# Kernel tuning notes

Hardware: AMD Instinct MI355X
Metric: run time of the kernel (lower is better)

## Reference

```python
import jax, jax.numpy as jnp
import numpy as np

MB, NK, DM, DT = 4096, 8, 1024, 128
EPS = 1e-3  # LayerNormalization eps, added to sigma OUTSIDE sqrt


def setup_inputs() -> dict:
    key = jax.random.key(0)
    ks = jax.random.split(key, 7)
    xav = lambda fan_in, fan_out: (2.0 / (fan_in + fan_out)) ** 0.5
    return {
        "q": jax.random.normal(ks[0], (MB, NK, DM), jnp.float32),
        "k": jax.random.normal(ks[1], (MB, NK, DM), jnp.float32),
        "v": jax.random.normal(ks[2], (MB, NK, DM), jnp.float32),
        "w_qs": jax.random.normal(ks[3], (NK, DM, DT), jnp.float32) * xav(DM, DT),
        "w_ks": jax.random.normal(ks[4], (NK, DM, DT), jnp.float32) * xav(DM, DT),
        "w_vs": jax.random.normal(ks[5], (NK, DM, DT), jnp.float32) * xav(DM, DT),
        # torch Linear: weight [out, in] = [NK*DM, NK*DT]
        "proj_w": jax.random.normal(ks[6], (NK * DM, NK * DT), jnp.float32) * xav(NK * DT, NK * DM),
        "proj_b": jnp.zeros((NK * DM,), jnp.float32),
        "gamma": jnp.ones((DM,), jnp.float32),
        "beta": jnp.zeros((DM,), jnp.float32),
    }


def reference(q, k, v, w_qs, w_ks, w_vs, proj_w, proj_b, gamma, beta):
    mb, nk, dm = q.shape
    dt = w_qs.shape[-1]
    residual = v

    # torch: q.view(n_kernel, mb, d_model) on contiguous [mb, nk, dm] == raw reshape
    q_s = jnp.einsum('nbd,ndt->nbt', q.reshape(nk, mb, dm), w_qs)  # [nk, mb, dt]
    k_s = jnp.einsum('nbd,ndt->nbt', k.reshape(nk, mb, dm), w_ks)
    v_s = jnp.einsum('nbd,ndt->nbt', v.reshape(nk, mb, dm), w_vs)

    # ScaledDotProductAttention on [nk*mb, 1, dt] -> scores [.,1,1]; softmax over
    # a singleton dim is identically 1, so output == v_s (faithful to source).
    temper = np.float32(np.sqrt(dm))
    scores = jnp.sum(q_s * k_s, axis=-1) / temper            # [nk, mb]
    attn = jax.nn.softmax(scores[:, :, None, None], axis=-1)  # [nk, mb, 1, 1] == 1.0
    out = attn[..., 0] * v_s                                  # [nk, mb, dt]
    attns = attn.reshape(nk * mb, 1, 1)

    # torch .view(mb, nk*dt) on the [nk, mb, dt]-contiguous buffer (raw reshape)
    outputs = out.reshape(mb, nk * dt)
    outputs = outputs @ proj_w.T + proj_b                     # [mb, nk*dm]
    z = outputs.reshape(mb, nk, dm) + residual

    # custom LayerNormalization: unbiased std, eps outside sqrt
    mu = jnp.mean(z, axis=-1, keepdims=True)
    sigma = jnp.std(z, axis=-1, keepdims=True, ddof=1)
    output = (z - mu) / (sigma + EPS) * gamma + beta
    return (output, attns)
```

## Files before the change

### kernel.cpp

```cpp
#include <hip/hip_runtime.h>
#include <cstdint>
#include <cstddef>

#define MB_   4096
#define NK_   8
#define DM_   1024
#define DT_   128

typedef __bf16 bf16;
typedef __bf16 bf16x8 __attribute__((ext_vector_type(8)));
typedef __bf16 bf16x4 __attribute__((ext_vector_type(4)));
typedef float  f32x4  __attribute__((ext_vector_type(4)));

__device__ __forceinline__ void gload_lds16(const void* g, void* l) {
  __builtin_amdgcn_global_load_lds(
      (__attribute__((address_space(1))) void*)g,
      (__attribute__((address_space(3))) void*)l,
      16, 0, 0);
}

__device__ __forceinline__ int hsw(int r) { return (r ^ (r >> 2)) & 3; }

__global__ void prep_pw_kernel(const float* __restrict__ pw, bf16* __restrict__ pwb) {
  size_t i = ((size_t)blockIdx.x * 256 + threadIdx.x) * 4;
  float4 f = *(const float4*)&pw[i];
  bf16x4 o = { (bf16)f.x, (bf16)f.y, (bf16)f.z, (bf16)f.w };
  *(bf16x4*)&pwb[i] = o;
}

__global__ void prep_wvt_kernel(const float* __restrict__ wvs, bf16* __restrict__ wvt) {
  int o = blockIdx.x * 256 + threadIdx.x;
  int d = o & 1023;
  int t = (o >> 10) & 127;
  int n = o >> 17;
  wvt[o] = (bf16)wvs[(size_t)n * 131072 + (size_t)d * 128 + t];
}

__global__ void fill_attns_kernel(float* __restrict__ out) {
  out[(size_t)33554432 + blockIdx.x * 256 + threadIdx.x] = 1.0f;
}

__global__ __launch_bounds__(256, 2) void gemm1_kernel(
    const float* __restrict__ vflat, const bf16* __restrict__ WvT,
    bf16* __restrict__ A2)
{
  __shared__ __align__(16) bf16 As[64 * 32];
  __shared__ __align__(16) bf16 Bs[128 * 32];
  const int tid  = threadIdx.x;
  const int wave = tid >> 6, lane = tid & 63;
  const int wm = wave >> 1, wn = wave & 1;
  const int n  = blockIdx.y;
  const int b0 = blockIdx.x * 64;

  const int r  = tid >> 2;
  const int hr = hsw(r);
  const int cs = (tid & 3) ^ hr;

  const float* ag = vflat + ((size_t)(n * MB_ + b0 + r)) * 1024 + (tid & 3) * 8;
  bf16* awr = As + r * 32 + cs * 8;
  const bf16* bg = WvT + (size_t)n * 131072 + (size_t)r * 1024 + cs * 8;
  char* bsb = (char*)Bs + wave * 1024;

  f32x4 acc[2][4] = {};
  const int krow = lane & 15;
  const int cch  = lane >> 4;
  const int swoff = ((cch ^ hsw(krow)) << 4);

  for (int kt = 0; kt < 32; ++kt) {
    const bf16* bptr = bg + kt * 32;
    gload_lds16(bptr,             bsb);
    gload_lds16(bptr + 64 * 1024, bsb + 4096);
    const float* aptr = ag + kt * 32;
    float4 f0 = *(const float4*)(aptr + 0);
    float4 f1 = *(const float4*)(aptr + 4);
    bf16x8 h0 = { (bf16)f0.x, (bf16)f0.y, (bf16)f0.z, (bf16)f0.w,
                  (bf16)f1.x, (bf16)f1.y, (bf16)f1.z, (bf16)f1.w };
    *(bf16x8*)awr = h0;
    __syncthreads();

    bf16x8 af[2], bfr[4];
    #pragma unroll
    for (int i = 0; i < 2; ++i)
      af[i] = *(const bf16x8*)((const char*)As + (wm * 32 + i * 16 + krow) * 64 + swoff);
    #pragma unroll
    for (int j = 0; j < 4; ++j)
      bfr[j] = *(const bf16x8*)((const char*)Bs + (wn * 64 + j * 16 + krow) * 64 + swoff);
    #pragma unroll
    for (int i = 0; i < 2; ++i)
      #pragma unroll
      for (int j = 0; j < 4; ++j)
        acc[i][j] = __builtin_amdgcn_mfma_f32_16x16x32_bf16(af[i], bfr[j], acc[i][j], 0, 0, 0);
    __syncthreads();
  }

  #pragma unroll
  for (int i = 0; i < 2; ++i) {
    #pragma unroll
    for (int j = 0; j < 4; ++j) {
      int t = wn * 64 + j * 16 + (lane & 15);
      #pragma unroll
      for (int rr = 0; rr < 4; ++rr) {
        int b = b0 + wm * 32 + i * 16 + (lane >> 4) * 4 + rr;
        size_t off = ((size_t)(n * 512 + (b >> 3))) * 1024 + (size_t)(b & 7) * 128 + t;
        A2[off] = (bf16)acc[i][j][rr];
      }
    }
  }
}

template<bool ZB>
__global__ __launch_bounds__(256, 2) void gemm2_kernel(
    const bf16* __restrict__ A2, const bf16* __restrict__ PW,
    const float* __restrict__ pb, void* __restrict__ zoutp)
{
  __shared__ __align__(16) bf16 As[128 * 32];
  __shared__ __align__(16) bf16 Bs[128 * 32];
  const int tid  = threadIdx.x;
  const int wave = tid >> 6, lane = tid & 63;
  const int wm = wave >> 1, wn = wave & 1;
  const int m0 = blockIdx.y * 128;
  const int n0 = blockIdx.x * 128;

  const int r  = tid >> 2;
  const int hr = hsw(r);
  const int cs = (tid & 3) ^ hr;

  const bf16* ag = A2 + (size_t)(m0 + r) * 1024 + cs * 8;
  const bf16* bg = PW + (size_t)(n0 + r) * 1024 + cs * 8;
  char* asb = (char*)As + wave * 1024;
  char* bsb = (char*)Bs + wave * 1024;

  f32x4 acc[4][4] = {};
  const int krow = lane & 15;
  const int cch  = lane >> 4;
  const int swoff = ((cch ^ hsw(krow)) << 4);

  for (int kt = 0; kt < 32; ++kt) {
    const bf16* a0 = ag + kt * 32;
    const bf16* b0 = bg + kt * 32;
    gload_lds16(a0,             asb);
    gload_lds16(a0 + 64 * 1024, asb + 4096);
    gload_lds16(b0,             bsb);
    gload_lds16(b0 + 64 * 1024, bsb + 4096);
    __syncthreads();

    bf16x8 af[4], bfr[4];
    #pragma unroll
    for (int i = 0; i < 4; ++i)
      af[i] = *(const bf16x8*)((const char*)As + (wm * 64 + i * 16 + krow) * 64 + swoff);
    #pragma unroll
    for (int j = 0; j < 4; ++j)
      bfr[j] = *(const bf16x8*)((const char*)Bs + (wn * 64 + j * 16 + krow) * 64 + swoff);
    #pragma unroll
    for (int i = 0; i < 4; ++i)
      #pragma unroll
      for (int j = 0; j < 4; ++j)
        acc[i][j] = __builtin_amdgcn_mfma_f32_16x16x32_bf16(af[i], bfr[j], acc[i][j], 0, 0, 0);
    __syncthreads();
  }

  #pragma unroll
  for (int i = 0; i < 4; ++i) {
    #pragma unroll
    for (int j = 0; j < 4; ++j) {
      int nn = n0 + wn * 64 + j * 16 + (lane & 15);
      float pbn = pb[nn];
      #pragma unroll
      for (int rr = 0; rr < 4; ++rr) {
        int mm = m0 + wm * 64 + i * 16 + (lane >> 4) * 4 + rr;
        size_t off = (size_t)mm * 8192 + nn;
        float val = acc[i][j][rr] + pbn;
        if (ZB) ((bf16*)zoutp)[off] = (bf16)val;
        else    ((float*)zoutp)[off] = val;
      }
    }
  }
}

template<bool ZB>
__global__ __launch_bounds__(256) void ln_kernel(
    const void* zin, const float* __restrict__ vres,
    const float* __restrict__ gamma, const float* __restrict__ beta,
    float* outp)
{
  __shared__ float red[16];
  const int row = blockIdx.x;
  const int tid = threadIdx.x;
  const size_t base = (size_t)row * 1024 + tid * 4;

  float4 rv = *(const float4*)&vres[base];
  float4 x;
  if (ZB) {
    bf16x4 zb4 = *(const bf16x4*)((const bf16*)zin + base);
    x.x = (float)zb4[0] + rv.x; x.y = (float)zb4[1] + rv.y;
    x.z = (float)zb4[2] + rv.z; x.w = (float)zb4[3] + rv.w;
  } else {
    float4 zf = *(const float4*)((const float*)zin + base);
    x.x = zf.x + rv.x; x.y = zf.y + rv.y; x.z = zf.z + rv.z; x.w = zf.w + rv.w;
  }

  float s  = x.x + x.y + x.z + x.w;
  float ss = x.x * x.x + x.y * x.y + x.z * x.z + x.w * x.w;
  #pragma unroll
  for (int m = 32; m >= 1; m >>= 1) {
    s  += __shfl_xor(s,  m, 64);
    ss += __shfl_xor(ss, m, 64);
  }
  const int wave = tid >> 6, lane = tid & 63;
  if (lane == 0) { red[wave] = s; red[wave + 8] = ss; }
  __syncthreads();
  float S  = red[0] + red[1] + red[2] + red[3];
  float SS = red[8] + red[9] + red[10] + red[11];
  float mu  = S * (1.0f / 1024.0f);
  float var = (SS - 1024.0f * mu * mu) * (1.0f / 1023.0f);
  var = var < 0.0f ? 0.0f : var;
  float rs = 1.0f / (sqrtf(var) + 1e-3f);
  float4 g  = *(const float4*)&gamma[tid * 4];
  float4 be = *(const float4*)&beta[tid * 4];
  float4 y;
  y.x = (x.x - mu) * rs * g.x + be.x;
  y.y = (x.y - mu) * rs * g.y + be.y;
  y.z = (x.z - mu) * rs * g.z + be.z;
  y.w = (x.w - mu) * rs * g.w + be.w;
  *(float4*)&outp[base] = y;
}

extern "C" void kernel_launch(void* const* d_in, const int* in_sizes, int n_in,
                              void* d_out, int out_size, void* d_ws, size_t ws_size,
                              hipStream_t stream) {
  const float* v     = (const float*)d_in[2];
  const float* wvs   = (const float*)d_in[5];
  const float* pw    = (const float*)d_in[6];
  const float* pb    = (const float*)d_in[7];
  const float* gamma = (const float*)d_in[8];
  const float* beta  = (const float*)d_in[9];
  float* out = (float*)d_out;

  const size_t OFF_WVT = 16777216;
  const size_t OFF_A2  = OFF_WVT + 2097152;
  const size_t OFF_ZG  = OFF_A2 + 8388608;
  const size_t NEED_ZB = OFF_ZG + 67108864;

  bf16* PWb = (bf16*)d_ws;
  bf16* WvT = (bf16*)((char*)d_ws + OFF_WVT);
  bf16* A2  = (bf16*)((char*)d_ws + OFF_A2);
  const bool zb = (ws_size >= NEED_ZB);
  void* zbuf = zb ? (void*)((char*)d_ws + OFF_ZG) : (void*)out;

  hipLaunchKernelGGL(prep_pw_kernel,    dim3(8192), dim3(256), 0, stream, pw, PWb);
  hipLaunchKernelGGL(prep_wvt_kernel,   dim3(4096), dim3(256), 0, stream, wvs, WvT);
  hipLaunchKernelGGL(fill_attns_kernel, dim3(128),  dim3(256), 0, stream, out);
  hipLaunchKernelGGL(gemm1_kernel, dim3(64, 8), dim3(256), 0, stream, v, WvT, A2);
  if (zb) {
    hipLaunchKernelGGL((gemm2_kernel<true>),  dim3(64, 32), dim3(256), 0, stream, A2, PWb, pb, zbuf);
    hipLaunchKernelGGL((ln_kernel<true>),     dim3(32768),  dim3(256), 0, stream, zbuf, v, gamma, beta, out);
  } else {
    hipLaunchKernelGGL((gemm2_kernel<false>), dim3(64, 32), dim3(256), 0, stream, A2, PWb, pb, zbuf);
    hipLaunchKernelGGL((ln_kernel<false>),    dim3(32768),  dim3(256), 0, stream, zbuf, v, gamma, beta, out);
  }
}
```

Before: 204.2 us.

## Fuse output projection GEMM with residual add and LayerNorm epilogue

```diff
diff --git a/kernel.cpp b/kernel.cpp
--- a/kernel.cpp
+++ b/kernel.cpp
@@ -108,121 +108,138 @@
   }
 }
 
-template<bool ZB>
-__global__ __launch_bounds__(256, 2) void gemm2_kernel(
+__global__ __launch_bounds__(512, 2) void gemm2ln_kernel(
     const bf16* __restrict__ A2, const bf16* __restrict__ PW,
-    const float* __restrict__ pb, void* __restrict__ zoutp)
+    const float* __restrict__ vres, const float* __restrict__ pb,
+    const float* __restrict__ gamma, const float* __restrict__ beta,
+    float* __restrict__ outp)
 {
-  __shared__ __align__(16) bf16 As[128 * 32];
-  __shared__ __align__(16) bf16 Bs[128 * 32];
+  __shared__ __align__(16) bf16 As[2][64 * 32];
+  __shared__ __align__(16) bf16 Bs[2][1024 * 32];
+  __shared__ float sred[2][64][8];
+
   const int tid  = threadIdx.x;
-  const int wave = tid >> 6, lane = tid & 63;
-  const int wm = wave >> 1, wn = wave & 1;
-  const int m0 = blockIdx.y * 128;
-  const int n0 = blockIdx.x * 128;
-
-  const int r  = tid >> 2;
-  const int hr = hsw(r);
-  const int cs = (tid & 3) ^ hr;
-
-  const bf16* ag = A2 + (size_t)(m0 + r) * 1024 + cs * 8;
-  const bf16* bg = PW + (size_t)(n0 + r) * 1024 + cs * 8;
-  char* asb = (char*)As + wave * 1024;
-  char* bsb = (char*)Bs + wave * 1024;
-
-  f32x4 acc[4][4] = {};
+  const int w    = tid >> 6;
+  const int lane = tid & 63;
+
+  const int bid = blockIdx.x;
+  const int j   = bid & 7;
+  const int m0  = (bid >> 3) * 64;
+  const int nc0 = j * 1024;
+
+  const int ra = tid >> 2;
+  const int ca = (tid & 3) ^ hsw(ra);
+  const bf16* aSrc = A2 + (size_t)(m0 + ra) * 1024 + ca * 8;
+  int bOff[8];
+  #pragma unroll
+  for (int q = 0; q < 8; ++q) {
+    int s  = q * 512 + tid;
+    int rb = s >> 2;
+    int cb = (s & 3) ^ hsw(rb);
+    bOff[q] = (nc0 + rb) * 1024 + cb * 8;
+  }
+
+  f32x4 acc[4][8] = {};
   const int krow = lane & 15;
   const int cch  = lane >> 4;
   const int swoff = ((cch ^ hsw(krow)) << 4);
 
-  for (int kt = 0; kt < 32; ++kt) {
-    const bf16* a0 = ag + kt * 32;
-    const bf16* b0 = bg + kt * 32;
-    gload_lds16(a0,             asb);
-    gload_lds16(a0 + 64 * 1024, asb + 4096);
-    gload_lds16(b0,             bsb);
-    gload_lds16(b0 + 64 * 1024, bsb + 4096);
+  {
+    #pragma unroll
+    for (int q = 0; q < 8; ++q)
+      gload_lds16(PW + bOff[q], (char*)Bs[0] + q * 8192 + w * 1024);
+    if (w < 4) gload_lds16(aSrc, (char*)As[0] + w * 1024);
+  }
+  __syncthreads();
+
+  for (int t = 0; t < 32; ++t) {
+    const int cur = t & 1;
+    if (t < 31) {
+      const int k0 = (t + 1) * 32;
+      #pragma unroll
+      for (int q = 0; q < 8; ++q)
+        gload_lds16(PW + bOff[q] + k0, (char*)Bs[cur ^ 1] + q * 8192 + w * 1024);
+      if (w < 4) gload_lds16(aSrc + k0, (char*)As[cur ^ 1] + w * 1024);
+    }
+    bf16x8 af[4], bfr[8];
+    #pragma unroll
+    for (int i = 0; i < 4; ++i)
+      af[i] = *(const bf16x8*)((const char*)As[cur] + (i * 16 + krow) * 64 + swoff);
+    #pragma unroll
+    for (int n = 0; n < 8; ++n)
+      bfr[n] = *(const bf16x8*)((const char*)Bs[cur] + (w * 128 + n * 16 + krow) * 64 + swoff);
+    #pragma unroll
+    for (int i = 0; i < 4; ++i)
+      #pragma unroll
+      for (int n = 0; n < 8; ++n)
+        acc[i][n] = __builtin_amdgcn_mfma_f32_16x16x32_bf16(af[i], bfr[n], acc[i][n], 0, 0, 0);
     __syncthreads();
-
-    bf16x8 af[4], bfr[4];
+  }
+
+  const int g = lane >> 4, q16 = lane & 15;
+  float pbv[8], gav[8], bev[8];
+  #pragma unroll
+  for (int n = 0; n < 8; ++n) {
+    int c = w * 128 + n * 16 + q16;
+    pbv[n] = pb[nc0 + c];
+    gav[n] = gamma[c];
+    bev[n] = beta[c];
+  }
+  #pragma unroll
+  for (int i = 0; i < 4; ++i) {
+    #pragma unroll
+    for (int r = 0; r < 4; ++r) {
+      int row = m0 + i * 16 + g * 4 + r;
+      const float* vrow = vres + (size_t)row * 8192 + nc0 + w * 128 + q16;
+      #pragma unroll
+      for (int n = 0; n < 8; ++n)
+        acc[i][n][r] += pbv[n] + vrow[n * 16];
+    }
+  }
+  float sv[16], qv[16];
+  #pragma unroll
+  for (int i = 0; i < 4; ++i) {
+    #pragma unroll
+    for (int r = 0; r < 4; ++r) {
+      float s = 0.0f, q2 = 0.0f;
+      #pragma unroll
+      for (int n = 0; n < 8; ++n) { float x = acc[i][n][r]; s += x; q2 += x * x; }
+      #pragma unroll
+      for (int m = 8; m >= 1; m >>= 1) {
+        s  += __shfl_xor(s,  m, 64);
+        q2 += __shfl_xor(q2, m, 64);
+      }
+      sv[i * 4 + r] = s; qv[i * 4 + r] = q2;
+    }
+  }
+  if (q16 == 0) {
     #pragma unroll
     for (int i = 0; i < 4; ++i)
-      af[i] = *(const bf16x8*)((const char*)As + (wm * 64 + i * 16 + krow) * 64 + swoff);
-    #pragma unroll
-    for (int j = 0; j < 4; ++j)
-      bfr[j] = *(const bf16x8*)((const char*)Bs + (wn * 64 + j * 16 + krow) * 64 + swoff);
-    #pragma unroll
-    for (int i = 0; i < 4; ++i)
-      #pragma unroll
-      for (int j = 0; j < 4; ++j)
-        acc[i][j] = __builtin_amdgcn_mfma_f32_16x16x32_bf16(af[i], bfr[j], acc[i][j], 0, 0, 0);
-    __syncthreads();
-  }
-
+      #pragma unroll
+      for (int r = 0; r < 4; ++r) {
+        sred[0][i * 16 + g * 4 + r][w] = sv[i * 4 + r];
+        sred[1][i * 16 + g * 4 + r][w] = qv[i * 4 + r];
+      }
+  }
+  __syncthreads();
   #pragma unroll
   for (int i = 0; i < 4; ++i) {
     #pragma unroll
-    for (int j = 0; j < 4; ++j) {
-      int nn = n0 + wn * 64 + j * 16 + (lane & 15);
-      float pbn = pb[nn];
-      #pragma unroll
-      for (int rr = 0; rr < 4; ++rr) {
-        int mm = m0 + wm * 64 + i * 16 + (lane >> 4) * 4 + rr;
-        size_t off = (size_t)mm * 8192 + nn;
-        float val = acc[i][j][rr] + pbn;
-        if (ZB) ((bf16*)zoutp)[off] = (bf16)val;
-        else    ((float*)zoutp)[off] = val;
-      }
-    }
-  }
-}
-
-template<bool ZB>
-__global__ __launch_bounds__(256) void ln_kernel(
-    const void* zin, const float* __restrict__ vres,
-    const float* __restrict__ gamma, const float* __restrict__ beta,
-    float* outp)
-{
-  __shared__ float red[16];
-  const int row = blockIdx.x;
-  const int tid = threadIdx.x;
-  const size_t base = (size_t)row * 1024 + tid * 4;
-
-  float4 rv = *(const float4*)&vres[base];
-  float4 x;
-  if (ZB) {
-    bf16x4 zb4 = *(const bf16x4*)((const bf16*)zin + base);
-    x.x = (float)zb4[0] + rv.x; x.y = (float)zb4[1] + rv.y;
-    x.z = (float)zb4[2] + rv.z; x.w = (float)zb4[3] + rv.w;
-  } else {
-    float4 zf = *(const float4*)((const float*)zin + base);
-    x.x = zf.x + rv.x; x.y = zf.y + rv.y; x.z = zf.z + rv.z; x.w = zf.w + rv.w;
-  }
-
-  float s  = x.x + x.y + x.z + x.w;
-  float ss = x.x * x.x + x.y * x.y + x.z * x.z + x.w * x.w;
-  #pragma unroll
-  for (int m = 32; m >= 1; m >>= 1) {
-    s  += __shfl_xor(s,  m, 64);
-    ss += __shfl_xor(ss, m, 64);
-  }
-  const int wave = tid >> 6, lane = tid & 63;
-  if (lane == 0) { red[wave] = s; red[wave + 8] = ss; }
-  __syncthreads();
-  float S  = red[0] + red[1] + red[2] + red[3];
-  float SS = red[8] + red[9] + red[10] + red[11];
-  float mu  = S * (1.0f / 1024.0f);
-  float var = (SS - 1024.0f * mu * mu) * (1.0f / 1023.0f);
-  var = var < 0.0f ? 0.0f : var;
-  float rs = 1.0f / (sqrtf(var) + 1e-3f);
-  float4 g  = *(const float4*)&gamma[tid * 4];
-  float4 be = *(const float4*)&beta[tid * 4];
-  float4 y;
-  y.x = (x.x - mu) * rs * g.x + be.x;
-  y.y = (x.y - mu) * rs * g.y + be.y;
-  y.z = (x.z - mu) * rs * g.z + be.z;
-  y.w = (x.w - mu) * rs * g.w + be.w;
-  *(float4*)&outp[base] = y;
+    for (int r = 0; r < 4; ++r) {
+      int lrow = i * 16 + g * 4 + r;
+      float S = 0.0f, SS = 0.0f;
+      #pragma unroll
+      for (int ww = 0; ww < 8; ++ww) { S += sred[0][lrow][ww]; SS += sred[1][lrow][ww]; }
+      float mu  = S * (1.0f / 1024.0f);
+      float var = (SS - 1024.0f * mu * mu) * (1.0f / 1023.0f);
+      var = var < 0.0f ? 0.0f : var;
+      float rs = 1.0f / (sqrtf(var) + 1e-3f);
+      float* orow = outp + (size_t)(m0 + lrow) * 8192 + nc0 + w * 128 + q16;
+      #pragma unroll
+      for (int n = 0; n < 8; ++n)
+        orow[n * 16] = (acc[i][n][r] - mu) * rs * gav[n] + bev[n];
+    }
+  }
 }
 
 extern "C" void kernel_launch(void* const* d_in, const int* in_sizes, int n_in,
@@ -238,24 +255,15 @@
 
   const size_t OFF_WVT = 16777216;
   const size_t OFF_A2  = OFF_WVT + 2097152;
-  const size_t OFF_ZG  = OFF_A2 + 8388608;
-  const size_t NEED_ZB = OFF_ZG + 67108864;
 
   bf16* PWb = (bf16*)d_ws;
   bf16* WvT = (bf16*)((char*)d_ws + OFF_WVT);
   bf16* A2  = (bf16*)((char*)d_ws + OFF_A2);
-  const bool zb = (ws_size >= NEED_ZB);
-  void* zbuf = zb ? (void*)((char*)d_ws + OFF_ZG) : (void*)out;
 
   hipLaunchKernelGGL(prep_pw_kernel,    dim3(8192), dim3(256), 0, stream, pw, PWb);
   hipLaunchKernelGGL(prep_wvt_kernel,   dim3(4096), dim3(256), 0, stream, wvs, WvT);
   hipLaunchKernelGGL(fill_attns_kernel, dim3(128),  dim3(256), 0, stream, out);
-  hipLaunchKernelGGL(gemm1_kernel, dim3(64, 8), dim3(256), 0, stream, v, WvT, A2);
-  if (zb) {
-    hipLaunchKernelGGL((gemm2_kernel<true>),  dim3(64, 32), dim3(256), 0, stream, A2, PWb, pb, zbuf);
-    hipLaunchKernelGGL((ln_kernel<true>),     dim3(32768),  dim3(256), 0, stream, zbuf, v, gamma, beta, out);
-  } else {
-    hipLaunchKernelGGL((gemm2_kernel<false>), dim3(64, 32), dim3(256), 0, stream, A2, PWb, pb, zbuf);
-    hipLaunchKernelGGL((ln_kernel<false>),    dim3(32768),  dim3(256), 0, stream, zbuf, v, gamma, beta, out);
-  }
-}
+  hipLaunchKernelGGL(gemm1_kernel,  dim3(64, 8), dim3(256), 0, stream, v, WvT, A2);
+  hipLaunchKernelGGL(gemm2ln_kernel, dim3(512),  dim3(512), 0, stream,
+                     A2, PWb, v, pb, gamma, beta, out);
+}
```

Result: slower. 213.0 us (+4.3%).

## Rewrite projection GEMM with 256x256 tiles and 4-stage LDS pipeline

Applied to the files above, without the earlier changes.

```diff
diff --git a/kernel.cpp b/kernel.cpp
--- a/kernel.cpp
+++ b/kernel.cpp
@@ -109,67 +109,102 @@
 }
 
 template<bool ZB>
-__global__ __launch_bounds__(256, 2) void gemm2_kernel(
+__global__ __launch_bounds__(512, 2) void gemm2p_kernel(
     const bf16* __restrict__ A2, const bf16* __restrict__ PW,
     const float* __restrict__ pb, void* __restrict__ zoutp)
 {
-  __shared__ __align__(16) bf16 As[128 * 32];
-  __shared__ __align__(16) bf16 Bs[128 * 32];
+  __shared__ __align__(16) bf16 As[4][8192];
+  __shared__ __align__(16) bf16 Bs[4][8192];
+
   const int tid  = threadIdx.x;
-  const int wave = tid >> 6, lane = tid & 63;
-  const int wm = wave >> 1, wn = wave & 1;
-  const int m0 = blockIdx.y * 128;
-  const int n0 = blockIdx.x * 128;
-
-  const int r  = tid >> 2;
-  const int hr = hsw(r);
-  const int cs = (tid & 3) ^ hr;
-
-  const bf16* ag = A2 + (size_t)(m0 + r) * 1024 + cs * 8;
-  const bf16* bg = PW + (size_t)(n0 + r) * 1024 + cs * 8;
-  char* asb = (char*)As + wave * 1024;
-  char* bsb = (char*)Bs + wave * 1024;
-
-  f32x4 acc[4][4] = {};
-  const int krow = lane & 15;
-  const int cch  = lane >> 4;
-  const int swoff = ((cch ^ hsw(krow)) << 4);
-
-  for (int kt = 0; kt < 32; ++kt) {
-    const bf16* a0 = ag + kt * 32;
-    const bf16* b0 = bg + kt * 32;
-    gload_lds16(a0,             asb);
-    gload_lds16(a0 + 64 * 1024, asb + 4096);
-    gload_lds16(b0,             bsb);
-    gload_lds16(b0 + 64 * 1024, bsb + 4096);
-    __syncthreads();
-
-    bf16x8 af[4], bfr[4];
-    #pragma unroll
-    for (int i = 0; i < 4; ++i)
-      af[i] = *(const bf16x8*)((const char*)As + (wm * 64 + i * 16 + krow) * 64 + swoff);
-    #pragma unroll
-    for (int j = 0; j < 4; ++j)
-      bfr[j] = *(const bf16x8*)((const char*)Bs + (wn * 64 + j * 16 + krow) * 64 + swoff);
-    #pragma unroll
-    for (int i = 0; i < 4; ++i)
-      #pragma unroll
-      for (int j = 0; j < 4; ++j)
-        acc[i][j] = __builtin_amdgcn_mfma_f32_16x16x32_bf16(af[i], bfr[j], acc[i][j], 0, 0, 0);
-    __syncthreads();
-  }
+  const int w    = tid >> 6;
+  const int lane = tid & 63;
+  const int wm   = w >> 2;
+  const int wn   = w & 3;
+
+  const int bid   = blockIdx.x;
+  const int x     = bid & 7;
+  const int local = bid >> 3;
+  const int mt    = local & 15;
+  const int nt    = x * 4 + (local >> 4);
+  const int m0    = mt * 256;
+  const int n0    = nt * 256;
+
+  const char* aG0 = (const char*)A2 + (size_t)(m0 + (tid >> 2)) * 2048 + (tid & 3) * 16;
+  const char* aG1 = aG0 + (size_t)128 * 2048;
+  const char* bG0 = (const char*)PW + (size_t)(n0 + (tid >> 2)) * 2048 + (tid & 3) * 16;
+  const char* bG1 = bG0 + (size_t)128 * 2048;
+
+  #define STAGE_A(t) { char* d = (char*)As[(t) & 3] + tid * 16;            \
+                       gload_lds16(aG0 + (t) * 64, d);                      \
+                       gload_lds16(aG1 + (t) * 64, d + 8192); }
+  #define STAGE_B(t) { char* d = (char*)Bs[(t) & 3] + tid * 16;            \
+                       gload_lds16(bG0 + (t) * 64, d);                      \
+                       gload_lds16(bG1 + (t) * 64, d + 8192); }
+
+  STAGE_A(0); STAGE_B(0); STAGE_A(1); STAGE_B(1);
+  asm volatile("s_waitcnt vmcnt(4)" ::: "memory");
+  __builtin_amdgcn_sched_barrier(0);
+  __builtin_amdgcn_s_barrier();
+
+  f32x4 acc[8][4] = {};
+  const int fr = lane & 15;
+  const int kc = (lane >> 4) * 8;
+  const int aRd = (wm * 128 + fr) * 32 + kc;
+  const int bRd = (wn * 64  + fr) * 32 + kc;
+
+  #pragma unroll 4
+  for (int t = 0; t < 32; ++t) {
+    const bf16* pA = &As[t & 3][aRd];
+    const bf16* pB = &Bs[t & 3][bRd];
+
+    bf16x8 a[4], b[4];
+    #pragma unroll
+    for (int m = 0; m < 4; ++m) a[m] = *(const bf16x8*)(pA + m * 512);
+    #pragma unroll
+    for (int n = 0; n < 4; ++n) b[n] = *(const bf16x8*)(pB + n * 512);
+    if (t < 30) STAGE_A(t + 2);
+    __builtin_amdgcn_s_barrier();
+    __builtin_amdgcn_s_setprio(1);
+    #pragma unroll
+    for (int m = 0; m < 4; ++m)
+      #pragma unroll
+      for (int n = 0; n < 4; ++n)
+        acc[m][n] = __builtin_amdgcn_mfma_f32_16x16x32_bf16(a[m], b[n], acc[m][n], 0, 0, 0);
+    __builtin_amdgcn_s_setprio(0);
+    __builtin_amdgcn_s_barrier();
+
+    bf16x8 a2[4];
+    #pragma unroll
+    for (int m = 0; m < 4; ++m) a2[m] = *(const bf16x8*)(pA + (4 + m) * 512);
+    if (t < 30) STAGE_B(t + 2);
+    __builtin_amdgcn_s_barrier();
+    __builtin_amdgcn_s_setprio(1);
+    #pragma unroll
+    for (int m = 0; m < 4; ++m)
+      #pragma unroll
+      for (int n = 0; n < 4; ++n)
+        acc[4 + m][n] = __builtin_amdgcn_mfma_f32_16x16x32_bf16(a2[m], b[n], acc[4 + m][n], 0, 0, 0);
+    __builtin_amdgcn_s_setprio(0);
+    if (t < 30)       { asm volatile("s_waitcnt vmcnt(4)" ::: "memory"); }
+    else if (t == 30) { asm volatile("s_waitcnt vmcnt(0)" ::: "memory"); }
+    __builtin_amdgcn_sched_barrier(0);
+    __builtin_amdgcn_s_barrier();
+  }
+  #undef STAGE_A
+  #undef STAGE_B
 
   #pragma unroll
-  for (int i = 0; i < 4; ++i) {
-    #pragma unroll
-    for (int j = 0; j < 4; ++j) {
-      int nn = n0 + wn * 64 + j * 16 + (lane & 15);
+  for (int m = 0; m < 8; ++m) {
+    #pragma unroll
+    for (int n = 0; n < 4; ++n) {
+      int nn = n0 + wn * 64 + n * 16 + fr;
       float pbn = pb[nn];
       #pragma unroll
-      for (int rr = 0; rr < 4; ++rr) {
-        int mm = m0 + wm * 64 + i * 16 + (lane >> 4) * 4 + rr;
+      for (int r = 0; r < 4; ++r) {
+        int mm = m0 + wm * 128 + m * 16 + (lane >> 4) * 4 + r;
         size_t off = (size_t)mm * 8192 + nn;
-        float val = acc[i][j][rr] + pbn;
+        float val = acc[m][n][r] + pbn;
         if (ZB) ((bf16*)zoutp)[off] = (bf16)val;
         else    ((float*)zoutp)[off] = val;
       }
@@ -252,10 +287,10 @@
   hipLaunchKernelGGL(fill_attns_kernel, dim3(128),  dim3(256), 0, stream, out);
   hipLaunchKernelGGL(gemm1_kernel, dim3(64, 8), dim3(256), 0, stream, v, WvT, A2);
   if (zb) {
-    hipLaunchKernelGGL((gemm2_kernel<true>),  dim3(64, 32), dim3(256), 0, stream, A2, PWb, pb, zbuf);
-    hipLaunchKernelGGL((ln_kernel<true>),     dim3(32768),  dim3(256), 0, stream, zbuf, v, gamma, beta, out);
+    hipLaunchKernelGGL((gemm2p_kernel<true>),  dim3(512), dim3(512), 0, stream, A2, PWb, pb, zbuf);
+    hipLaunchKernelGGL((ln_kernel<true>),      dim3(32768), dim3(256), 0, stream, zbuf, v, gamma, beta, out);
   } else {
-    hipLaunchKernelGGL((gemm2_kernel<false>), dim3(64, 32), dim3(256), 0, stream, A2, PWb, pb, zbuf);
-    hipLaunchKernelGGL((ln_kernel<false>),    dim3(32768),  dim3(256), 0, stream, zbuf, v, gamma, beta, out);
-  }
-}
+    hipLaunchKernelGGL((gemm2p_kernel<false>), dim3(512), dim3(512), 0, stream, A2, PWb, pb, zbuf);
+    hipLaunchKernelGGL((ln_kernel<false>),     dim3(32768), dim3(256), 0, stream, zbuf, v, gamma, beta, out);
+  }
+}
```

Measured after the change: 202.6 us. No clear change (-0.8%).
